# Performance work log

Hardware: AMD Instinct MI355X
Metric: run time of the kernel (lower is better)

Reference implementation:

```python
import jax, jax.numpy as jnp
import numpy as np

BS, LX, LY, H, MD = 16, 1024, 1024, 512, 512


def setup_inputs() -> dict:
    key = jax.random.key(0)
    ks = jax.random.split(key, 8)
    x = jax.random.normal(ks[0], (BS, LX, H), dtype=jnp.float32)
    y = jax.random.normal(ks[1], (BS, LY, H), dtype=jnp.float32)
    y_mask = jax.random.bernoulli(ks[2], 0.2, (BS, LY))  # True = masked
    s1 = 1.0 / np.sqrt(H)
    W1 = jax.random.uniform(ks[3], (MD, H), jnp.float32, -s1, s1)
    b1 = jax.random.uniform(ks[4], (MD,), jnp.float32, -s1, s1)
    W2 = jax.random.uniform(ks[5], (MD, H), jnp.float32, -s1, s1)
    b2 = jax.random.uniform(ks[6], (MD,), jnp.float32, -s1, s1)
    s2 = 1.0 / np.sqrt(MD)
    k7, k8 = jax.random.split(ks[7])
    w_o = jax.random.uniform(k7, (MD,), jnp.float32, -s2, s2)
    b_o = jax.random.uniform(k8, (), jnp.float32, -s2, s2)
    return {"x": x, "y": y, "y_mask": y_mask, "W1": W1, "b1": b1,
            "W2": W2, "b2": b2, "w_o": w_o, "b_o": b_o}


def reference(x, y, y_mask, W1, b1, W2, b2, w_o, b_o):
    # Projections: [B,L,MD]
    x_proj = jax.nn.relu(jnp.einsum('blh,mh->blm', x, W1) + b1)
    y_proj = jax.nn.relu(jnp.einsum('blh,mh->blm', y, W2) + b2)
    # o_liner is linear, so o_liner(x_i + y_j) = w_o.x_i + w_o.y_j + b_o
    sx = x_proj @ w_o  # [B,Lx]
    sy = y_proj @ w_o  # [B,Ly]
    scores = sx[:, :, None] + sy[:, None, :] + b_o  # [B,Lx,Ly]
    scores = jnp.where(y_mask[:, None, :], jnp.float32(-1e7), scores)
    alpha = jax.nn.softmax(scores, axis=-1)  # softmax over len_y
    return alpha
```

## Files before the change

### kernel.cpp

```cpp
#include <hip/hip_runtime.h>
#include <hip/hip_bf16.h>

#define BS 16
#define LX 1024
#define LY 1024
#define H 512
#define MD 512
#define RY (BS * LY)

typedef __attribute__((ext_vector_type(8))) __bf16 bf16x8;
typedef __attribute__((ext_vector_type(4))) float floatx4;

__device__ __forceinline__ void load_lds16(const __bf16* g, __bf16* l) {
    __builtin_amdgcn_global_load_lds(
        (const __attribute__((address_space(1))) void*)g,
        (__attribute__((address_space(3))) void*)l,
        16, 0, 0);
}

__global__ __launch_bounds__(256) void prep_w2(const float* __restrict__ W2,
                                               __bf16* __restrict__ wb) {
    const int i = blockIdx.x * 256 + threadIdx.x;
    const float4 a = *(const float4*)(W2 + (size_t)i * 8);
    const float4 b = *(const float4*)(W2 + (size_t)i * 8 + 4);
    bf16x8 v = { (__bf16)a.x, (__bf16)a.y, (__bf16)a.z, (__bf16)a.w,
                 (__bf16)b.x, (__bf16)b.y, (__bf16)b.z, (__bf16)b.w };
    *(bf16x8*)(wb + (size_t)i * 8) = v;
}

#define BM 64
#define BN 128
#define BKT 64
#define ASTR 72
__global__ __launch_bounds__(256) void gemm_sy(const float* __restrict__ Y,
                                               const __bf16* __restrict__ wb,
                                               const float* __restrict__ b2,
                                               const float* __restrict__ wo,
                                               float* __restrict__ part) {
    __shared__ __align__(16) __bf16 As[BM * ASTR];
    __shared__ __align__(16) __bf16 Bs[BN * BKT];

    const int tid  = threadIdx.x;
    const int lane = tid & 63;
    const int wave = tid >> 6;
    const int wm = wave >> 1;
    const int wn = wave & 1;
    const int la = lane & 15;
    const int qa = lane >> 4;

    const int id = blockIdx.x;
    const int mt = ((id >> 5) << 3) | (id & 7);
    const int nt = (id >> 3) & 3;
    const int m0 = mt * BM, n0 = nt * BN;

    const int lrow = lane >> 3;
    const int lcol = ((lane & 7) ^ lrow) * 8;

    const int ar = tid >> 2;
    const int ac = (tid & 3) * 16;
    const float* ybase = Y + (size_t)(m0 + ar) * H + ac;

    floatx4 acc[2][4] = {};

    for (int k0 = 0; k0 < H; k0 += BKT) {
        __syncthreads();
        #pragma unroll
        for (int r = 0; r < 4; ++r) {
            const int rb = r * 32 + wave * 8;
            load_lds16(wb + (size_t)(n0 + rb + lrow) * H + k0 + lcol, &Bs[rb * BKT]);
        }
        const float4 a0 = *(const float4*)(ybase + k0);
        const float4 a1 = *(const float4*)(ybase + k0 + 4);
        const float4 a2 = *(const float4*)(ybase + k0 + 8);
        const float4 a3 = *(const float4*)(ybase + k0 + 12);
        bf16x8 p0 = { (__bf16)a0.x, (__bf16)a0.y, (__bf16)a0.z, (__bf16)a0.w,
                      (__bf16)a1.x, (__bf16)a1.y, (__bf16)a1.z, (__bf16)a1.w };
        bf16x8 p1 = { (__bf16)a2.x, (__bf16)a2.y, (__bf16)a2.z, (__bf16)a2.w,
                      (__bf16)a3.x, (__bf16)a3.y, (__bf16)a3.z, (__bf16)a3.w };
        *(bf16x8*)&As[ar * ASTR + ac]     = p0;
        *(bf16x8*)&As[ar * ASTR + ac + 8] = p1;
        __syncthreads();

        #pragma unroll
        for (int kh = 0; kh < 2; ++kh) {
            bf16x8 afr[2], bfr[4];
            #pragma unroll
            for (int mf = 0; mf < 2; ++mf)
                afr[mf] = *(const bf16x8*)&As[(wm * 32 + mf * 16 + la) * ASTR + kh * 32 + qa * 8];
            #pragma unroll
            for (int nf = 0; nf < 4; ++nf) {
                const int row  = wn * 64 + nf * 16 + la;
                const int slot = (kh * 4 + qa) ^ (la & 7);
                bfr[nf] = *(const bf16x8*)&Bs[row * BKT + slot * 8];
            }
            #pragma unroll
            for (int mf = 0; mf < 2; ++mf)
                #pragma unroll
                for (int nf = 0; nf < 4; ++nf)
                    acc[mf][nf] = __builtin_amdgcn_mfma_f32_16x16x32_bf16(afr[mf], bfr[nf], acc[mf][nf], 0, 0, 0);
        }
    }

    const int slice = nt * 2 + wn;
    #pragma unroll
    for (int mf = 0; mf < 2; ++mf) {
        #pragma unroll
        for (int reg = 0; reg < 4; ++reg) {
            float s = 0.f;
            #pragma unroll
            for (int nf = 0; nf < 4; ++nf) {
                const int n = n0 + wn * 64 + nf * 16 + la;
                float v = acc[mf][nf][reg] + b2[n];
                v = fmaxf(v, 0.f);
                s += v * wo[n];
            }
            s += __shfl_xor(s, 1);
            s += __shfl_xor(s, 2);
            s += __shfl_xor(s, 4);
            s += __shfl_xor(s, 8);
            if (la == 0) {
                const int m = m0 + wm * 32 + mf * 16 + qa * 4 + reg;
                part[(size_t)slice * RY + m] = s;
            }
        }
    }
}

__global__ __launch_bounds__(256) void softmax_p(const float* __restrict__ part,
                                                 const int* __restrict__ mask,
                                                 float* __restrict__ p) {
    const int b = blockIdx.x;
    const int tid = threadIdx.x;
    __shared__ float red[8];

    float vals[4];
    int   ms[4];
    float mx = -INFINITY;
    #pragma unroll
    for (int c = 0; c < 4; ++c) {
        const int j = c * 256 + tid;
        float v = 0.f;
        #pragma unroll
        for (int t = 0; t < 8; ++t) v += part[t * RY + b * LY + j];
        vals[c] = v;
        ms[c]   = mask[b * LY + j];
        if (!ms[c]) mx = fmaxf(mx, v);
    }
    #pragma unroll
    for (int off = 1; off < 64; off <<= 1) mx = fmaxf(mx, __shfl_xor(mx, off));
    if ((tid & 63) == 0) red[tid >> 6] = mx;
    __syncthreads();
    mx = fmaxf(fmaxf(red[0], red[1]), fmaxf(red[2], red[3]));

    float e[4];
    float sum = 0.f;
    #pragma unroll
    for (int c = 0; c < 4; ++c) {
        e[c] = ms[c] ? 0.f : __expf(vals[c] - mx);
        sum += e[c];
    }
    #pragma unroll
    for (int off = 1; off < 64; off <<= 1) sum += __shfl_xor(sum, off);
    if ((tid & 63) == 0) red[4 + (tid >> 6)] = sum;
    __syncthreads();
    sum = red[4] + red[5] + red[6] + red[7];
    const float inv = 1.0f / sum;

    #pragma unroll
    for (int c = 0; c < 4; ++c)
        p[b * LY + c * 256 + tid] = e[c] * inv;
}

__global__ __launch_bounds__(256) void bcast(const float* __restrict__ p,
                                             float4* __restrict__ out) {
    const int tid = threadIdx.x;
    const long base_row = (long)blockIdx.x * 8;
    const int b = (int)(base_row >> 10);
    const float4 v = *(const float4*)(p + b * LY + tid * 4);
    float4* o = out + base_row * (LY / 4) + tid;
    #pragma unroll
    for (int r = 0; r < 8; ++r) o[r * (LY / 4)] = v;
}

extern "C" void kernel_launch(void* const* d_in, const int* in_sizes, int n_in,
                              void* d_out, int out_size, void* d_ws, size_t ws_size,
                              hipStream_t stream) {
    const float* y  = (const float*)d_in[1];
    const int*   ym = (const int*)  d_in[2];
    const float* W2 = (const float*)d_in[5];
    const float* b2 = (const float*)d_in[6];
    const float* wo = (const float*)d_in[7];

    char* ws = (char*)d_ws;
    __bf16* wb   = (__bf16*)ws;
    float*  part = (float*)(ws + (size_t)MD * H * 2);
    float*  p    = part + 8 * RY;

    prep_w2<<<(MD * H) / (256 * 8), 256, 0, stream>>>(W2, wb);
    gemm_sy<<<(MD / BN) * (RY / BM), 256, 0, stream>>>(y, wb, b2, wo, part);
    softmax_p<<<BS, 256, 0, stream>>>(part, ym, p);
    bcast<<<(BS * LX) / 8, 256, 0, stream>>>(p, (float4*)d_out);
}
```

Baseline: 146.5 us.

## Double-buffer GEMM tiles with larger M tile and fuse softmax into broadcast

The sy GEMM tile grows from 64 to 128 rows per block, and the B tile in LDS is double-buffered, so the next K slice's weight and Y loads are issued while MFMAs run on the current slice. The separate softmax kernel and broadcast kernel become one kernel in which every output block recomputes the per-batch softmax from the partial sums before writing its rows. This removes a launch and the intermediate p buffer. In exchange, each softmax is computed redundantly 128 times, and the GEMM grid has half as many blocks while using more registers.

```diff
diff --git a/kernel.cpp b/kernel.cpp
--- a/kernel.cpp
+++ b/kernel.cpp
@@ -28,17 +28,17 @@
     *(bf16x8*)(wb + (size_t)i * 8) = v;
 }
 
-#define BM 64
+#define BM 128
 #define BN 128
 #define BKT 64
 #define ASTR 72
-__global__ __launch_bounds__(256) void gemm_sy(const float* __restrict__ Y,
-                                               const __bf16* __restrict__ wb,
-                                               const float* __restrict__ b2,
-                                               const float* __restrict__ wo,
-                                               float* __restrict__ part) {
+__global__ __launch_bounds__(256, 2) void gemm_sy(const float* __restrict__ Y,
+                                                  const __bf16* __restrict__ wb,
+                                                  const float* __restrict__ b2,
+                                                  const float* __restrict__ wo,
+                                                  float* __restrict__ part) {
     __shared__ __align__(16) __bf16 As[BM * ASTR];
-    __shared__ __align__(16) __bf16 Bs[BN * BKT];
+    __shared__ __align__(16) __bf16 Bs[2][BN * BKT];
 
     const int tid  = threadIdx.x;
     const int lane = tid & 63;
@@ -56,54 +56,78 @@
     const int lrow = lane >> 3;
     const int lcol = ((lane & 7) ^ lrow) * 8;
 
-    const int ar = tid >> 2;
-    const int ac = (tid & 3) * 16;
+    const int ar = tid >> 1;
+    const int ac = (tid & 1) * 32;
     const float* ybase = Y + (size_t)(m0 + ar) * H + ac;
 
-    floatx4 acc[2][4] = {};
-
-    for (int k0 = 0; k0 < H; k0 += BKT) {
-        __syncthreads();
-        #pragma unroll
-        for (int r = 0; r < 4; ++r) {
-            const int rb = r * 32 + wave * 8;
-            load_lds16(wb + (size_t)(n0 + rb + lrow) * H + k0 + lcol, &Bs[rb * BKT]);
-        }
-        const float4 a0 = *(const float4*)(ybase + k0);
-        const float4 a1 = *(const float4*)(ybase + k0 + 4);
-        const float4 a2 = *(const float4*)(ybase + k0 + 8);
-        const float4 a3 = *(const float4*)(ybase + k0 + 12);
-        bf16x8 p0 = { (__bf16)a0.x, (__bf16)a0.y, (__bf16)a0.z, (__bf16)a0.w,
-                      (__bf16)a1.x, (__bf16)a1.y, (__bf16)a1.z, (__bf16)a1.w };
-        bf16x8 p1 = { (__bf16)a2.x, (__bf16)a2.y, (__bf16)a2.z, (__bf16)a2.w,
-                      (__bf16)a3.x, (__bf16)a3.y, (__bf16)a3.z, (__bf16)a3.w };
-        *(bf16x8*)&As[ar * ASTR + ac]     = p0;
-        *(bf16x8*)&As[ar * ASTR + ac + 8] = p1;
-        __syncthreads();
+    floatx4 acc[4][4] = {};
+
+    #pragma unroll
+    for (int r = 0; r < 4; ++r) {
+        const int rb = r * 32 + wave * 8;
+        load_lds16(wb + (size_t)(n0 + rb + lrow) * H + 0 + lcol, &Bs[0][rb * BKT]);
+    }
+    {
+        float4 a0[8];
+        #pragma unroll
+        for (int j = 0; j < 8; ++j) a0[j] = *(const float4*)(ybase + j * 4);
+        #pragma unroll
+        for (int i = 0; i < 4; ++i) {
+            bf16x8 p = { (__bf16)a0[2*i].x, (__bf16)a0[2*i].y, (__bf16)a0[2*i].z, (__bf16)a0[2*i].w,
+                         (__bf16)a0[2*i+1].x, (__bf16)a0[2*i+1].y, (__bf16)a0[2*i+1].z, (__bf16)a0[2*i+1].w };
+            *(bf16x8*)&As[ar * ASTR + ac + i * 8] = p;
+        }
+    }
+    __syncthreads();
+
+    for (int t = 0; t < 8; ++t) {
+        const int buf = t & 1;
+        float4 nxt[8];
+        if (t < 7) {
+            const int k0 = (t + 1) * BKT;
+            #pragma unroll
+            for (int r = 0; r < 4; ++r) {
+                const int rb = r * 32 + wave * 8;
+                load_lds16(wb + (size_t)(n0 + rb + lrow) * H + k0 + lcol, &Bs[buf ^ 1][rb * BKT]);
+            }
+            #pragma unroll
+            for (int j = 0; j < 8; ++j) nxt[j] = *(const float4*)(ybase + k0 + j * 4);
+        }
 
         #pragma unroll
         for (int kh = 0; kh < 2; ++kh) {
-            bf16x8 afr[2], bfr[4];
-            #pragma unroll
-            for (int mf = 0; mf < 2; ++mf)
-                afr[mf] = *(const bf16x8*)&As[(wm * 32 + mf * 16 + la) * ASTR + kh * 32 + qa * 8];
+            bf16x8 afr[4], bfr[4];
+            #pragma unroll
+            for (int mf = 0; mf < 4; ++mf)
+                afr[mf] = *(const bf16x8*)&As[(wm * 64 + mf * 16 + la) * ASTR + kh * 32 + qa * 8];
             #pragma unroll
             for (int nf = 0; nf < 4; ++nf) {
                 const int row  = wn * 64 + nf * 16 + la;
                 const int slot = (kh * 4 + qa) ^ (la & 7);
-                bfr[nf] = *(const bf16x8*)&Bs[row * BKT + slot * 8];
-            }
-            #pragma unroll
-            for (int mf = 0; mf < 2; ++mf)
+                bfr[nf] = *(const bf16x8*)&Bs[buf][row * BKT + slot * 8];
+            }
+            #pragma unroll
+            for (int mf = 0; mf < 4; ++mf)
                 #pragma unroll
                 for (int nf = 0; nf < 4; ++nf)
                     acc[mf][nf] = __builtin_amdgcn_mfma_f32_16x16x32_bf16(afr[mf], bfr[nf], acc[mf][nf], 0, 0, 0);
         }
+
+        __syncthreads();
+        if (t < 7) {
+            #pragma unroll
+            for (int i = 0; i < 4; ++i) {
+                bf16x8 p = { (__bf16)nxt[2*i].x, (__bf16)nxt[2*i].y, (__bf16)nxt[2*i].z, (__bf16)nxt[2*i].w,
+                             (__bf16)nxt[2*i+1].x, (__bf16)nxt[2*i+1].y, (__bf16)nxt[2*i+1].z, (__bf16)nxt[2*i+1].w };
+                *(bf16x8*)&As[ar * ASTR + ac + i * 8] = p;
+            }
+        }
+        __syncthreads();
     }
 
     const int slice = nt * 2 + wn;
     #pragma unroll
-    for (int mf = 0; mf < 2; ++mf) {
+    for (int mf = 0; mf < 4; ++mf) {
         #pragma unroll
         for (int reg = 0; reg < 4; ++reg) {
             float s = 0.f;
@@ -119,67 +143,57 @@
             s += __shfl_xor(s, 4);
             s += __shfl_xor(s, 8);
             if (la == 0) {
-                const int m = m0 + wm * 32 + mf * 16 + qa * 4 + reg;
+                const int m = m0 + wm * 64 + mf * 16 + qa * 4 + reg;
                 part[(size_t)slice * RY + m] = s;
             }
         }
     }
 }
 
-__global__ __launch_bounds__(256) void softmax_p(const float* __restrict__ part,
-                                                 const int* __restrict__ mask,
-                                                 float* __restrict__ p) {
-    const int b = blockIdx.x;
+__global__ __launch_bounds__(256) void softmax_bcast(const float* __restrict__ part,
+                                                     const int* __restrict__ mask,
+                                                     float4* __restrict__ out) {
     const int tid = threadIdx.x;
+    const long base_row = (long)blockIdx.x * 8;
+    const int b = (int)(base_row >> 10);
     __shared__ float red[8];
 
-    float vals[4];
-    int   ms[4];
+    float4 v = {0.f, 0.f, 0.f, 0.f};
+    #pragma unroll
+    for (int t = 0; t < 8; ++t) {
+        const float4 q = *(const float4*)(part + (size_t)t * RY + b * LY + tid * 4);
+        v.x += q.x; v.y += q.y; v.z += q.z; v.w += q.w;
+    }
+    const int4 m4 = *(const int4*)(mask + b * LY + tid * 4);
+
     float mx = -INFINITY;
-    #pragma unroll
-    for (int c = 0; c < 4; ++c) {
-        const int j = c * 256 + tid;
-        float v = 0.f;
-        #pragma unroll
-        for (int t = 0; t < 8; ++t) v += part[t * RY + b * LY + j];
-        vals[c] = v;
-        ms[c]   = mask[b * LY + j];
-        if (!ms[c]) mx = fmaxf(mx, v);
-    }
+    if (!m4.x) mx = v.x;
+    if (!m4.y) mx = fmaxf(mx, v.y);
+    if (!m4.z) mx = fmaxf(mx, v.z);
+    if (!m4.w) mx = fmaxf(mx, v.w);
     #pragma unroll
     for (int off = 1; off < 64; off <<= 1) mx = fmaxf(mx, __shfl_xor(mx, off));
     if ((tid & 63) == 0) red[tid >> 6] = mx;
     __syncthreads();
     mx = fmaxf(fmaxf(red[0], red[1]), fmaxf(red[2], red[3]));
 
-    float e[4];
-    float sum = 0.f;
-    #pragma unroll
-    for (int c = 0; c < 4; ++c) {
-        e[c] = ms[c] ? 0.f : __expf(vals[c] - mx);
-        sum += e[c];
-    }
+    float4 e;
+    e.x = m4.x ? 0.f : __expf(v.x - mx);
+    e.y = m4.y ? 0.f : __expf(v.y - mx);
+    e.z = m4.z ? 0.f : __expf(v.z - mx);
+    e.w = m4.w ? 0.f : __expf(v.w - mx);
+    float sum = e.x + e.y + e.z + e.w;
     #pragma unroll
     for (int off = 1; off < 64; off <<= 1) sum += __shfl_xor(sum, off);
     if ((tid & 63) == 0) red[4 + (tid >> 6)] = sum;
     __syncthreads();
     sum = red[4] + red[5] + red[6] + red[7];
     const float inv = 1.0f / sum;
-
-    #pragma unroll
-    for (int c = 0; c < 4; ++c)
-        p[b * LY + c * 256 + tid] = e[c] * inv;
-}
-
-__global__ __launch_bounds__(256) void bcast(const float* __restrict__ p,
-                                             float4* __restrict__ out) {
-    const int tid = threadIdx.x;
-    const long base_row = (long)blockIdx.x * 8;
-    const int b = (int)(base_row >> 10);
-    const float4 v = *(const float4*)(p + b * LY + tid * 4);
+    e.x *= inv; e.y *= inv; e.z *= inv; e.w *= inv;
+
     float4* o = out + base_row * (LY / 4) + tid;
     #pragma unroll
-    for (int r = 0; r < 8; ++r) o[r * (LY / 4)] = v;
+    for (int r = 0; r < 8; ++r) o[r * (LY / 4)] = e;
 }
 
 extern "C" void kernel_launch(void* const* d_in, const int* in_sizes, int n_in,
@@ -194,10 +208,8 @@
     char* ws = (char*)d_ws;
     __bf16* wb   = (__bf16*)ws;
     float*  part = (float*)(ws + (size_t)MD * H * 2);
-    float*  p    = part + 8 * RY;
 
     prep_w2<<<(MD * H) / (256 * 8), 256, 0, stream>>>(W2, wb);
     gemm_sy<<<(MD / BN) * (RY / BM), 256, 0, stream>>>(y, wb, b2, wo, part);
-    softmax_p<<<BS, 256, 0, stream>>>(part, ym, p);
-    bcast<<<(BS * LX) / 8, 256, 0, stream>>>(p, (float4*)d_out);
-}
+    softmax_bcast<<<(BS * LX) / 8, 256, 0, stream>>>(part, ym, (float4*)d_out);
+}
```

Result: slower. 152.0 us (+3.8%).

## Fuse softmax into broadcast kernel with nontemporal stores

Applied to the files above, without the earlier changes.

Merges the per-batch softmax kernel into the broadcast kernel. Each block of 16 output rows recomputes the softmax for its batch from the partial sums and mask, then writes the rows with nontemporal stores. This removes one launch and the intermediate probability buffer, and the softmax no longer runs on only 16 blocks. The cost is that the small softmax (reads of the partial sums plus two block reductions) is repeated 64 times per batch, and each block now writes 16 rows instead of 8.

```diff
diff --git a/kernel.cpp b/kernel.cpp
--- a/kernel.cpp
+++ b/kernel.cpp
@@ -126,60 +126,51 @@
     }
 }
 
-__global__ __launch_bounds__(256) void softmax_p(const float* __restrict__ part,
-                                                 const int* __restrict__ mask,
-                                                 float* __restrict__ p) {
-    const int b = blockIdx.x;
+__global__ __launch_bounds__(256) void softmax_bcast(const float* __restrict__ part,
+                                                     const int* __restrict__ mask,
+                                                     floatx4* __restrict__ out) {
     const int tid = threadIdx.x;
+    const long base_row = (long)blockIdx.x * 16;
+    const int b = (int)(base_row >> 10);
     __shared__ float red[8];
 
-    float vals[4];
-    int   ms[4];
+    float vx = 0.f, vy = 0.f, vz = 0.f, vw = 0.f;
+    #pragma unroll
+    for (int t = 0; t < 8; ++t) {
+        const float4 q = *(const float4*)(part + (size_t)t * RY + b * LY + tid * 4);
+        vx += q.x; vy += q.y; vz += q.z; vw += q.w;
+    }
+    const int4 m4 = *(const int4*)(mask + b * LY + tid * 4);
+
     float mx = -INFINITY;
-    #pragma unroll
-    for (int c = 0; c < 4; ++c) {
-        const int j = c * 256 + tid;
-        float v = 0.f;
-        #pragma unroll
-        for (int t = 0; t < 8; ++t) v += part[t * RY + b * LY + j];
-        vals[c] = v;
-        ms[c]   = mask[b * LY + j];
-        if (!ms[c]) mx = fmaxf(mx, v);
-    }
+    if (!m4.x) mx = vx;
+    if (!m4.y) mx = fmaxf(mx, vy);
+    if (!m4.z) mx = fmaxf(mx, vz);
+    if (!m4.w) mx = fmaxf(mx, vw);
     #pragma unroll
     for (int off = 1; off < 64; off <<= 1) mx = fmaxf(mx, __shfl_xor(mx, off));
     if ((tid & 63) == 0) red[tid >> 6] = mx;
     __syncthreads();
     mx = fmaxf(fmaxf(red[0], red[1]), fmaxf(red[2], red[3]));
 
-    float e[4];
-    float sum = 0.f;
-    #pragma unroll
-    for (int c = 0; c < 4; ++c) {
-        e[c] = ms[c] ? 0.f : __expf(vals[c] - mx);
-        sum += e[c];
-    }
+    floatx4 e;
+    e.x = m4.x ? 0.f : __expf(vx - mx);
+    e.y = m4.y ? 0.f : __expf(vy - mx);
+    e.z = m4.z ? 0.f : __expf(vz - mx);
+    e.w = m4.w ? 0.f : __expf(vw - mx);
+    float sum = e.x + e.y + e.z + e.w;
     #pragma unroll
     for (int off = 1; off < 64; off <<= 1) sum += __shfl_xor(sum, off);
     if ((tid & 63) == 0) red[4 + (tid >> 6)] = sum;
     __syncthreads();
     sum = red[4] + red[5] + red[6] + red[7];
     const float inv = 1.0f / sum;
+    e.x *= inv; e.y *= inv; e.z *= inv; e.w *= inv;
 
+    floatx4* o = out + base_row * (LY / 4) + tid;
     #pragma unroll
-    for (int c = 0; c < 4; ++c)
-        p[b * LY + c * 256 + tid] = e[c] * inv;
-}
-
-__global__ __launch_bounds__(256) void bcast(const float* __restrict__ p,
-                                             float4* __restrict__ out) {
-    const int tid = threadIdx.x;
-    const long base_row = (long)blockIdx.x * 8;
-    const int b = (int)(base_row >> 10);
-    const float4 v = *(const float4*)(p + b * LY + tid * 4);
-    float4* o = out + base_row * (LY / 4) + tid;
-    #pragma unroll
-    for (int r = 0; r < 8; ++r) o[r * (LY / 4)] = v;
+    for (int r = 0; r < 16; ++r)
+        __builtin_nontemporal_store(e, o + r * (LY / 4));
 }
 
 extern "C" void kernel_launch(void* const* d_in, const int* in_sizes, int n_in,
@@ -194,10 +185,8 @@
     char* ws = (char*)d_ws;
     __bf16* wb   = (__bf16*)ws;
     float*  part = (float*)(ws + (size_t)MD * H * 2);
-    float*  p    = part + 8 * RY;
 
     prep_w2<<<(MD * H) / (256 * 8), 256, 0, stream>>>(W2, wb);
     gemm_sy<<<(MD / BN) * (RY / BM), 256, 0, stream>>>(y, wb, b2, wo, part);
-    softmax_p<<<BS, 256, 0, stream>>>(part, ym, p);
-    bcast<<<(BS * LX) / 8, 256, 0, stream>>>(p, (float4*)d_out);
+    softmax_bcast<<<(BS * LX) / 16, 256, 0, stream>>>(part, ym, (floatx4*)d_out);
 }
```

Result: faster. 142.4 us, median of 2 (-2.8%).
